# Kernel tuning notes

Measured on AMD Instinct MI355X. Metric: run time of the kernel, lower is better.

## Reference

```python
import jax, jax.numpy as jnp
import numpy as np
from jax import lax

# ---- module hyperparams (match init_kwargs and mamba_ssm Mamba2 defaults) ----
D_MODEL = 768
D_STATE = 64
D_CONV = 4
EXPAND = 2
HEADDIM = 64  # Mamba2 default
D_INNER = EXPAND * D_MODEL          # 1536
NHEADS = D_INNER // HEADDIM         # 24
NGROUPS = 1
CONV_DIM = D_INNER + 2 * NGROUPS * D_STATE          # 1664
D_IN_PROJ = 2 * D_INNER + 2 * NGROUPS * D_STATE + NHEADS  # 3224
BSZ, SEQ = 2, 512
EPS = 1e-5


def setup_inputs() -> dict:
    key = jax.random.key(0)
    ks = jax.random.split(key, 12)
    def n(k, shape, s):
        return jax.random.normal(k, shape, jnp.float32) * s
    x = n(ks[0], (BSZ, SEQ, D_MODEL), 1.0)
    in_proj_w = n(ks[1], (D_IN_PROJ, D_MODEL), D_MODEL ** -0.5)
    conv_w = n(ks[2], (CONV_DIM, D_CONV), D_CONV ** -0.5)
    conv_b = jnp.zeros((CONV_DIM,), jnp.float32)
    # dt_bias = softplus^{-1}(dt) with dt log-uniform in [1e-3, 1e-1] (Mamba2 init)
    dt = jnp.exp(jax.random.uniform(ks[3], (NHEADS,), jnp.float32,
                                    minval=np.log(1e-3), maxval=np.log(1e-1)))
    dt_bias = dt + jnp.log(-jnp.expm1(-dt))
    A_log = jnp.log(jax.random.uniform(ks[4], (NHEADS,), jnp.float32, minval=1.0, maxval=16.0))
    D_param = jnp.ones((NHEADS,), jnp.float32)
    norm_w = jnp.ones((D_INNER,), jnp.float32)
    out_proj_w = n(ks[5], (D_MODEL, D_INNER), D_INNER ** -0.5)
    ln1_w = jnp.ones((D_MODEL,), jnp.float32); ln1_b = jnp.zeros((D_MODEL,), jnp.float32)
    ln2_w = jnp.ones((D_MODEL,), jnp.float32); ln2_b = jnp.zeros((D_MODEL,), jnp.float32)
    ff_w1 = n(ks[6], (4 * D_MODEL, D_MODEL), D_MODEL ** -0.5)
    ff_b1 = jnp.zeros((4 * D_MODEL,), jnp.float32)
    ff_w2 = n(ks[7], (D_MODEL, 4 * D_MODEL), (4 * D_MODEL) ** -0.5)
    ff_b2 = jnp.zeros((D_MODEL,), jnp.float32)
    return dict(x=x, in_proj_w=in_proj_w, conv_w=conv_w, conv_b=conv_b,
                dt_bias=dt_bias, A_log=A_log, D_param=D_param, norm_w=norm_w,
                out_proj_w=out_proj_w, ln1_w=ln1_w, ln1_b=ln1_b,
                ln2_w=ln2_w, ln2_b=ln2_b, ff_w1=ff_w1, ff_b1=ff_b1,
                ff_w2=ff_w2, ff_b2=ff_b2)


def layernorm(x, w, b):
    mu = jnp.mean(x, -1, keepdims=True)
    xc = x - mu
    var = jnp.mean(xc * xc, -1, keepdims=True)
    return xc * lax.rsqrt(var + EPS) * w + b


def mamba2(xn, in_proj_w, conv_w, conv_b, dt_bias, A_log, D_param, norm_w, out_proj_w):
    b, l, _ = xn.shape
    zxbcdt = xn @ in_proj_w.T  # [b, l, D_IN_PROJ]
    z = zxbcdt[..., :D_INNER]
    xBC = zxbcdt[..., D_INNER:D_INNER + CONV_DIM]
    dt = zxbcdt[..., D_INNER + CONV_DIM:]
    # causal depthwise conv over time on xBC
    xc = lax.conv_general_dilated(xBC.transpose(0, 2, 1), conv_w[:, None, :], (1,),
                                  [(D_CONV - 1, 0)], dimension_numbers=('NCH', 'OIH', 'NCH'),
                                  feature_group_count=CONV_DIM)
    xBC = jax.nn.silu((xc + conv_b[None, :, None]).transpose(0, 2, 1))
    xs = xBC[..., :D_INNER].reshape(b, l, NHEADS, HEADDIM)
    Bm = xBC[..., D_INNER:D_INNER + D_STATE]   # [b, l, n]  (ngroups=1)
    Cm = xBC[..., D_INNER + D_STATE:]          # [b, l, n]
    dt = jax.nn.softplus(dt + dt_bias)         # [b, l, h]
    dA = jnp.exp(dt * (-jnp.exp(A_log)))       # [b, l, h]
    dBx = jnp.einsum('blh,bln,blhp->blhpn', dt, Bm, xs)
    def step(h, inp):
        dA_t, dBx_t = inp                      # [b,h], [b,h,p,n]
        h = dA_t[:, :, None, None] * h + dBx_t
        return h, h
    _, hs = lax.scan(step, jnp.zeros((b, NHEADS, HEADDIM, D_STATE), xn.dtype),
                     (dA.transpose(1, 0, 2), dBx.transpose(1, 0, 2, 3, 4)))
    y = jnp.einsum('lbhpn,bln->blhp', hs, Cm) + D_param[None, None, :, None] * xs
    y = y.reshape(b, l, D_INNER) * jax.nn.silu(z)   # gated RMSNorm (norm_before_gate=False)
    y = y * lax.rsqrt(jnp.mean(y * y, -1, keepdims=True) + EPS) * norm_w
    return y @ out_proj_w.T


def reference(x, in_proj_w, conv_w, conv_b, dt_bias, A_log, D_param, norm_w,
              out_proj_w, ln1_w, ln1_b, ln2_w, ln2_b, ff_w1, ff_b1, ff_w2, ff_b2):
    residual = x
    xn = layernorm(x, ln1_w, ln1_b)
    mp = (in_proj_w, conv_w, conv_b, dt_bias, A_log, D_param, norm_w, out_proj_w)
    out_f = mamba2(xn, *mp)
    out_b = jnp.flip(mamba2(jnp.flip(xn, 1), *mp), 1)
    m = layernorm(out_f + out_b, ln2_w, ln2_b)
    ff = jax.nn.gelu(m @ ff_w1.T + ff_b1, approximate=False) @ ff_w2.T + ff_b2
    return ff + residual
```

## Files before the change

### kernel.cpp

```cpp
#include <hip/hip_runtime.h>
#include <hip/hip_bf16.h>
#include <math.h>

#define SEQ     512
#define BSZ     2
#define ROWS    (BSZ*SEQ)
#define DMODEL  768
#define DINNER  1536
#define DSTATE  64
#define NHEADS  24
#define HEADDIM 64
#define CONVDIM 1664
#define DINPROJ 3224
#define DFF     3072
#define EPSF    1e-5f

typedef __attribute__((ext_vector_type(8))) short s16x8;
typedef __attribute__((ext_vector_type(4))) float f32x4;

__device__ __forceinline__ float b2f(const __hip_bfloat16 v){ return __bfloat162float(v); }
__device__ __forceinline__ __hip_bfloat16 f2b(float v){ return __float2bfloat16(v); }
__device__ __forceinline__ ushort f2bu(float v){
  union { __hip_bfloat16 b; ushort u; } c; c.b = __float2bfloat16(v); return c.u;
}
__device__ __forceinline__ float u2f(ushort u){ return __uint_as_float(((uint)u) << 16); }

__device__ __forceinline__ void gload16(const void* g, void* l){
  __builtin_amdgcn_global_load_lds((__attribute__((address_space(1))) const void*)g,
                                   (__attribute__((address_space(3))) void*)l, 16, 0, 0);
}

__device__ __forceinline__ float block_sum256(float v, float* sh){
  #pragma unroll
  for (int off = 32; off > 0; off >>= 1) v += __shfl_down(v, off, 64);
  int w = threadIdx.x >> 6;
  if ((threadIdx.x & 63) == 0) sh[w] = v;
  __syncthreads();
  float t = sh[0] + sh[1] + sh[2] + sh[3];
  __syncthreads();
  return t;
}

__global__ __launch_bounds__(256) void zerof_kernel(float* out, int n){
  int i = blockIdx.x*256 + threadIdx.x;
  if (i < n) out[i] = 0.f;
}

__global__ __launch_bounds__(256) void w2b_kernel(const float* __restrict__ w,
    __hip_bfloat16* __restrict__ o, int n)
{
  int i = (blockIdx.x*256 + threadIdx.x) << 2;
  if (i >= n) return;
  float4 f = *(const float4*)(w + i);
  ushort4 u = make_ushort4(f2bu(f.x), f2bu(f.y), f2bu(f.z), f2bu(f.w));
  *(ushort4*)((ushort*)o + i) = u;
}

__global__ __launch_bounds__(256) void ln_kernel(const float* __restrict__ in,
    const float* __restrict__ w, const float* __restrict__ b,
    __hip_bfloat16* __restrict__ out)
{
  __shared__ float sh[4];
  const int row = blockIdx.x;
  const float* xr = in + (size_t)row * DMODEL;
  float v[3]; float s = 0.f;
  #pragma unroll
  for (int i = 0; i < 3; i++){ int c = threadIdx.x + i*256; v[i] = xr[c]; s += v[i]; }
  s = block_sum256(s, sh);
  float mu = s * (1.f/DMODEL);
  float s2 = 0.f;
  #pragma unroll
  for (int i = 0; i < 3; i++){ float d = v[i]-mu; s2 += d*d; }
  s2 = block_sum256(s2, sh);
  float rs = rsqrtf(s2*(1.f/DMODEL) + EPSF);
  #pragma unroll
  for (int i = 0; i < 3; i++){
    int c = threadIdx.x + i*256;
    out[(size_t)row*DMODEL + c] = f2b((v[i]-mu)*rs*w[c] + b[c]);
  }
}

__device__ __forceinline__ s16x8 ld_frag(const ushort* p){
  union { ushort4 h[2]; s16x8 v; } u;
  u.h[0] = *(const ushort4*)(p);
  u.h[1] = *(const ushort4*)(p + 4);
  return u.v;
}

template<typename CTy, int KS>
__global__ __launch_bounds__(256) void gemm_bb64(const __hip_bfloat16* __restrict__ A_,
    const __hip_bfloat16* __restrict__ B_, CTy* __restrict__ C, int M, int N, int K)
{
  __shared__ __align__(16) ushort As[2][64][64];
  __shared__ __align__(16) ushort Bs[2][64][64];
  const int tid  = threadIdx.x;
  const int lane = tid & 63, wave = tid >> 6;
  const int wr = wave >> 1, wc = wave & 1;
  const int n0 = blockIdx.x * 64, m0 = blockIdx.y * 64;
  const int Kc   = K / KS;
  const int kbeg = blockIdx.z * Kc;
  const int srw  = lane >> 3;
  const int scol = (((lane & 7) ^ srw) << 3);
  const int l15  = lane & 15;
  const int r7   = l15 & 7;
  const int c0   = lane >> 4;

  const ushort* Au = (const ushort*)A_;
  const ushort* Bu = (const ushort*)B_;

  f32x4 acc[2][2] = {};

  auto stage = [&](int bf, int k0){
    #pragma unroll
    for (int q = 0; q < 2; q++){
      int row = q*32 + wave*8 + srw;
      gload16(Au + (size_t)(m0 + row)*K + kbeg + k0 + scol, &As[bf][q*32 + wave*8][0]);
      int nr = n0 + row; if (nr > N-1) nr = N-1;
      gload16(Bu + (size_t)nr*K + kbeg + k0 + scol, &Bs[bf][q*32 + wave*8][0]);
    }
  };

  stage(0, 0);
  __syncthreads();
  int cur = 0;
  for (int k0 = 0; k0 < Kc; k0 += 64){
    if (k0 + 64 < Kc) stage(cur ^ 1, k0 + 64);
    #pragma unroll
    for (int t = 0; t < 2; t++){
      const int fc = (((t*4 + c0) ^ r7) << 3);
      s16x8 a0 = ld_frag(&As[cur][wr*32      + l15][fc]);
      s16x8 a1 = ld_frag(&As[cur][wr*32 + 16 + l15][fc]);
      s16x8 b0 = ld_frag(&Bs[cur][wc*32      + l15][fc]);
      s16x8 b1 = ld_frag(&Bs[cur][wc*32 + 16 + l15][fc]);
      acc[0][0] = __builtin_amdgcn_mfma_f32_16x16x32_bf16(a0, b0, acc[0][0], 0, 0, 0);
      acc[0][1] = __builtin_amdgcn_mfma_f32_16x16x32_bf16(a0, b1, acc[0][1], 0, 0, 0);
      acc[1][0] = __builtin_amdgcn_mfma_f32_16x16x32_bf16(a1, b0, acc[1][0], 0, 0, 0);
      acc[1][1] = __builtin_amdgcn_mfma_f32_16x16x32_bf16(a1, b1, acc[1][1], 0, 0, 0);
    }
    __syncthreads();
    cur ^= 1;
  }

  const int crow = (lane >> 4) * 4;
  #pragma unroll
  for (int i = 0; i < 2; i++){
    #pragma unroll
    for (int j = 0; j < 2; j++){
      int col = n0 + wc*32 + j*16 + l15;
      if (col < N){
        #pragma unroll
        for (int q = 0; q < 4; q++){
          int rowg = m0 + wr*32 + i*16 + crow + q;
          if constexpr (KS > 1) atomicAdd(&C[(size_t)rowg*N + col], acc[i][j][q]);
          else if constexpr (sizeof(CTy) == 4) C[(size_t)rowg*N + col] = acc[i][j][q];
          else C[(size_t)rowg*N + col] = (CTy)f2b(acc[i][j][q]);
        }
      }
    }
  }
}

template<typename CTy>
__global__ __launch_bounds__(256) void gemm_mfma(const __hip_bfloat16* __restrict__ A,
    const float* __restrict__ B, CTy* __restrict__ C, int M, int N, int K)
{
  __shared__ __align__(16) ushort As[64][72];
  __shared__ __align__(16) ushort Bs[64][72];
  const int tid  = threadIdx.x;
  const int lane = tid & 63, wave = tid >> 6;
  const int wr = wave >> 1, wc = wave & 1;
  const int n0 = blockIdx.x * 64, m0 = blockIdx.y * 64;
  const int sr = tid >> 2;
  const int sc = (tid & 3) * 16;
  const int l15 = lane & 15, lk = (lane >> 4) * 8;

  f32x4 acc[2][2] = {};

  const ushort* Au = (const ushort*)A;
  int nr = n0 + sr; if (nr > N-1) nr = N-1;

  for (int k0 = 0; k0 < K; k0 += 64){
    const ushort* ag = Au + (size_t)(m0 + sr)*K + (k0 + sc);
    ushort4 a0 = *(const ushort4*)(ag);
    ushort4 a1 = *(const ushort4*)(ag + 4);
    ushort4 a2 = *(const ushort4*)(ag + 8);
    ushort4 a3 = *(const ushort4*)(ag + 12);
    const float* bg = B + (size_t)nr*K + (k0 + sc);
    float4 f0 = *(const float4*)(bg);
    float4 f1 = *(const float4*)(bg + 4);
    float4 f2 = *(const float4*)(bg + 8);
    float4 f3 = *(const float4*)(bg + 12);
    ushort4 b0 = make_ushort4(f2bu(f0.x), f2bu(f0.y), f2bu(f0.z), f2bu(f0.w));
    ushort4 b1 = make_ushort4(f2bu(f1.x), f2bu(f1.y), f2bu(f1.z), f2bu(f1.w));
    ushort4 b2 = make_ushort4(f2bu(f2.x), f2bu(f2.y), f2bu(f2.z), f2bu(f2.w));
    ushort4 b3 = make_ushort4(f2bu(f3.x), f2bu(f3.y), f2bu(f3.z), f2bu(f3.w));

    __syncthreads();
    *(ushort4*)&As[sr][sc +  0] = a0;
    *(ushort4*)&As[sr][sc +  4] = a1;
    *(ushort4*)&As[sr][sc +  8] = a2;
    *(ushort4*)&As[sr][sc + 12] = a3;
    *(ushort4*)&Bs[sr][sc +  0] = b0;
    *(ushort4*)&Bs[sr][sc +  4] = b1;
    *(ushort4*)&Bs[sr][sc +  8] = b2;
    *(ushort4*)&Bs[sr][sc + 12] = b3;
    __syncthreads();

    #pragma unroll
    for (int kk = 0; kk < 64; kk += 32){
      s16x8 af0 = ld_frag(&As[wr*32      + l15][kk + lk]);
      s16x8 af1 = ld_frag(&As[wr*32 + 16 + l15][kk + lk]);
      s16x8 bf0 = ld_frag(&Bs[wc*32      + l15][kk + lk]);
      s16x8 bf1 = ld_frag(&Bs[wc*32 + 16 + l15][kk + lk]);
      acc[0][0] = __builtin_amdgcn_mfma_f32_16x16x32_bf16(af0, bf0, acc[0][0], 0, 0, 0);
      acc[0][1] = __builtin_amdgcn_mfma_f32_16x16x32_bf16(af0, bf1, acc[0][1], 0, 0, 0);
      acc[1][0] = __builtin_amdgcn_mfma_f32_16x16x32_bf16(af1, bf0, acc[1][0], 0, 0, 0);
      acc[1][1] = __builtin_amdgcn_mfma_f32_16x16x32_bf16(af1, bf1, acc[1][1], 0, 0, 0);
    }
  }

  const int crow = (lane >> 4) * 4;
  #pragma unroll
  for (int i = 0; i < 2; i++){
    #pragma unroll
    for (int j = 0; j < 2; j++){
      int col = n0 + wc*32 + j*16 + l15;
      if (col < N){
        #pragma unroll
        for (int q = 0; q < 4; q++){
          int rowg = m0 + wr*32 + i*16 + crow + q;
          if constexpr (sizeof(CTy) == 4) C[(size_t)rowg*N + col] = acc[i][j][q];
          else                            C[(size_t)rowg*N + col] = (CTy)f2b(acc[i][j][q]);
        }
      }
    }
  }
}

__global__ __launch_bounds__(256) void convdt_kernel(const __hip_bfloat16* __restrict__ zx,
    const float* __restrict__ cw, const float* __restrict__ cb,
    const float* __restrict__ dt_bias, const float* __restrict__ A_log,
    __hip_bfloat16* __restrict__ xconv, float* __restrict__ dtb, float* __restrict__ dab)
{
  const int tt = blockIdx.x, b = blockIdx.y, dir = blockIdx.z;
  size_t rowoff[4]; bool ok[4];
  #pragma unroll
  for (int k = 0; k < 4; k++){
    int s = tt - 3 + k;
    ok[k] = (s >= 0);
    int ss = ok[k] ? s : 0;
    int phys = dir ? (SEQ-1-ss) : ss;
    rowoff[k] = ((size_t)(b*SEQ + phys))*DINPROJ + DINNER;
  }
  __hip_bfloat16* outr = xconv + ((size_t)((dir*BSZ + b)*SEQ + tt))*CONVDIM;
  for (int c = threadIdx.x; c < CONVDIM; c += 256){
    float acc = cb[c];
    #pragma unroll
    for (int k = 0; k < 4; k++){
      if (ok[k]) acc += cw[c*4 + k] * b2f(zx[rowoff[k] + c]);
    }
    outr[c] = f2b(acc / (1.f + expf(-acc)));
  }
  if (dir == 0 && threadIdx.x < NHEADS){
    int h = threadIdx.x;
    size_t r = (size_t)b*SEQ + tt;
    float raw = b2f(zx[r*DINPROJ + (DINNER + CONVDIM) + h]) + dt_bias[h];
    float sp  = fmaxf(raw, 0.f) + log1pf(expf(-fabsf(raw)));
    dtb[r*NHEADS + h] = sp;
    dab[r*NHEADS + h] = expf(-sp * expf(A_log[h]));
  }
}

#define CT 16

__global__ __launch_bounds__(256) void scan_pass1(const __hip_bfloat16* __restrict__ xconv,
    const float* __restrict__ dtb, const float* __restrict__ dab,
    float* __restrict__ stateBuf, int CL)
{
  const int c = blockIdx.x, h = blockIdx.y, z = blockIdx.z;
  const int b = z & 1, dir = z >> 1;
  const int tid = threadIdx.x, lane = tid & 63, wave = tid >> 6, nb = wave * 16;
  __shared__ __align__(16) float Bc[CT][64], Xc[CT][64];
  __shared__ float dAc[CT], dtc[CT];
  float hreg[16];
  #pragma unroll
  for (int j = 0; j < 16; j++) hreg[j] = 0.f;
  const size_t dirbase = (size_t)z * SEQ;
  const int cstart = c * CL;

  const int ttl = tid >> 4, c4 = (tid & 15) << 2;

  for (int c0 = cstart; c0 < cstart + CL; c0 += CT){
    {
      const ushort* rowp = (const ushort*)xconv + (dirbase + c0 + ttl)*(size_t)CONVDIM;
      ushort4 bv = *(const ushort4*)(rowp + DINNER + c4);
      ushort4 xv = *(const ushort4*)(rowp + h*HEADDIM + c4);
      Bc[ttl][c4+0] = u2f(bv.x); Bc[ttl][c4+1] = u2f(bv.y);
      Bc[ttl][c4+2] = u2f(bv.z); Bc[ttl][c4+3] = u2f(bv.w);
      Xc[ttl][c4+0] = u2f(xv.x); Xc[ttl][c4+1] = u2f(xv.y);
      Xc[ttl][c4+2] = u2f(xv.z); Xc[ttl][c4+3] = u2f(xv.w);
    }
    if (tid < CT){
      int phys = dir ? (SEQ-1 - (c0 + tid)) : (c0 + tid);
      size_t r = (size_t)b*SEQ + phys;
      dAc[tid] = dab[r*NHEADS + h];
      dtc[tid] = dtb[r*NHEADS + h];
    }
    __syncthreads();

    #pragma unroll 4
    for (int tt = 0; tt < CT; tt++){
      float dA = dAc[tt];
      float dtx = dtc[tt] * Xc[tt][lane];
      const float4* Bq = (const float4*)&Bc[tt][nb];
      float4 B0 = Bq[0], B1 = Bq[1], B2 = Bq[2], B3 = Bq[3];
      hreg[ 0]=fmaf(dA,hreg[ 0],dtx*B0.x); hreg[ 1]=fmaf(dA,hreg[ 1],dtx*B0.y);
      hreg[ 2]=fmaf(dA,hreg[ 2],dtx*B0.z); hreg[ 3]=fmaf(dA,hreg[ 3],dtx*B0.w);
      hreg[ 4]=fmaf(dA,hreg[ 4],dtx*B1.x); hreg[ 5]=fmaf(dA,hreg[ 5],dtx*B1.y);
      hreg[ 6]=fmaf(dA,hreg[ 6],dtx*B1.z); hreg[ 7]=fmaf(dA,hreg[ 7],dtx*B1.w);
      hreg[ 8]=fmaf(dA,hreg[ 8],dtx*B2.x); hreg[ 9]=fmaf(dA,hreg[ 9],dtx*B2.y);
      hreg[10]=fmaf(dA,hreg[10],dtx*B2.z); hreg[11]=fmaf(dA,hreg[11],dtx*B2.w);
      hreg[12]=fmaf(dA,hreg[12],dtx*B3.x); hreg[13]=fmaf(dA,hreg[13],dtx*B3.y);
      hreg[14]=fmaf(dA,hreg[14],dtx*B3.z); hreg[15]=fmaf(dA,hreg[15],dtx*B3.w);
    }
    __syncthreads();
  }

  float* sp = stateBuf + (((size_t)c*4 + z)*NHEADS + h)*4096 + (size_t)lane*64 + nb;
  *(float4*)(sp +  0) = make_float4(hreg[ 0],hreg[ 1],hreg[ 2],hreg[ 3]);
  *(float4*)(sp +  4) = make_float4(hreg[ 4],hreg[ 5],hreg[ 6],hreg[ 7]);
  *(float4*)(sp +  8) = make_float4(hreg[ 8],hreg[ 9],hreg[10],hreg[11]);
  *(float4*)(sp + 12) = make_float4(hreg[12],hreg[13],hreg[14],hreg[15]);
}

__global__ __launch_bounds__(256) void scan_fixup(const float* __restrict__ dab,
    float* __restrict__ stateBuf, int NC, int CL)
{
  const int h = blockIdx.x, z = blockIdx.y;
  const int b = z & 1, dir = z >> 1;
  const int tid = threadIdx.x;
  __shared__ float sdA[SEQ];
  __shared__ float P[8];
  for (int i = tid; i < SEQ; i += 256){
    int phys = dir ? (SEQ-1-i) : i;
    sdA[i] = dab[((size_t)b*SEQ + phys)*NHEADS + h];
  }
  __syncthreads();
  if (tid < NC){
    float p = 1.f;
    for (int i = 0; i < CL; i++) p *= sdA[tid*CL + i];
    P[tid] = p;
  }
  __syncthreads();

  float hrun[16], Lcur[16];
  #pragma unroll
  for (int j = 0; j < 16; j++) hrun[j] = 0.f;
  {
    const float* s0 = stateBuf + ((size_t)z*NHEADS + h)*4096 + (size_t)tid*16;
    #pragma unroll
    for (int j = 0; j < 16; j++) Lcur[j] = s0[j];
  }
  for (int c = 1; c < NC; c++){
    float Pp = P[c-1];
    float hnew[16];
    #pragma unroll
    for (int j = 0; j < 16; j++) hnew[j] = fmaf(Pp, hrun[j], Lcur[j]);
    float* sc = stateBuf + (((size_t)c*4 + z)*NHEADS + h)*4096 + (size_t)tid*16;
    if (c < NC-1){
      #pragma unroll
      for (int j = 0; j < 16; j++) Lcur[j] = sc[j];
    }
    #pragma unroll
    for (int j = 0; j < 16; j++) sc[j] = hnew[j];
    #pragma unroll
    for (int j = 0; j < 16; j++) hrun[j] = hnew[j];
  }
}

__global__ __launch_bounds__(256) void scan_pass2(const __hip_bfloat16* __restrict__ xconv,
    const __hip_bfloat16* __restrict__ zx, const float* __restrict__ dtb,
    const float* __restrict__ dab, const float* __restrict__ Dp,
    const float* __restrict__ stateBuf, __hip_bfloat16* __restrict__ yg, int CL)
{
  const int c = blockIdx.x, h = blockIdx.y, z = blockIdx.z;
  const int b = z & 1, dir = z >> 1;
  const int tid = threadIdx.x, lane = tid & 63, wave = tid >> 6, nb = wave * 16;
  __shared__ __align__(16) float Bc[CT][64], Cc[CT][64], Xc[CT][64];
  __shared__ __align__(16) float Yp[4][CT][64];
  __shared__ float dAc[CT], dtc[CT];
  float hreg[16];
  if (c == 0){
    #pragma unroll
    for (int j = 0; j < 16; j++) hreg[j] = 0.f;
  } else {
    const float* sp = stateBuf + (((size_t)c*4 + z)*NHEADS + h)*4096 + (size_t)lane*64 + nb;
    float4 s0 = *(const float4*)(sp+0), s1 = *(const float4*)(sp+4);
    float4 s2 = *(const float4*)(sp+8), s3 = *(const float4*)(sp+12);
    hreg[ 0]=s0.x; hreg[ 1]=s0.y; hreg[ 2]=s0.z; hreg[ 3]=s0.w;
    hreg[ 4]=s1.x; hreg[ 5]=s1.y; hreg[ 6]=s1.z; hreg[ 7]=s1.w;
    hreg[ 8]=s2.x; hreg[ 9]=s2.y; hreg[10]=s2.z; hreg[11]=s2.w;
    hreg[12]=s3.x; hreg[13]=s3.y; hreg[14]=s3.z; hreg[15]=s3.w;
  }
  const float Dh = Dp[h];
  const size_t dirbase = (size_t)z * SEQ;
  const int cstart = c * CL;
  const int ttl = tid >> 4, c4 = (tid & 15) << 2;

  for (int c0 = cstart; c0 < cstart + CL; c0 += CT){
    {
      const ushort* rowp = (const ushort*)xconv + (dirbase + c0 + ttl)*(size_t)CONVDIM;
      ushort4 bv = *(const ushort4*)(rowp + DINNER + c4);
      ushort4 cv = *(const ushort4*)(rowp + DINNER + DSTATE + c4);
      ushort4 xv = *(const ushort4*)(rowp + h*HEADDIM + c4);
      Bc[ttl][c4+0] = u2f(bv.x); Bc[ttl][c4+1] = u2f(bv.y);
      Bc[ttl][c4+2] = u2f(bv.z); Bc[ttl][c4+3] = u2f(bv.w);
      Cc[ttl][c4+0] = u2f(cv.x); Cc[ttl][c4+1] = u2f(cv.y);
      Cc[ttl][c4+2] = u2f(cv.z); Cc[ttl][c4+3] = u2f(cv.w);
      Xc[ttl][c4+0] = u2f(xv.x); Xc[ttl][c4+1] = u2f(xv.y);
      Xc[ttl][c4+2] = u2f(xv.z); Xc[ttl][c4+3] = u2f(xv.w);
    }
    if (tid < CT){
      int phys = dir ? (SEQ-1 - (c0 + tid)) : (c0 + tid);
      size_t r = (size_t)b*SEQ + phys;
      dAc[tid] = dab[r*NHEADS + h];
      dtc[tid] = dtb[r*NHEADS + h];
    }
    __syncthreads();

    #pragma unroll 4
    for (int tt = 0; tt < CT; tt++){
      float dA = dAc[tt];
      float dtx = dtc[tt] * Xc[tt][lane];
      const float4* Bq = (const float4*)&Bc[tt][nb];
      const float4* Cq = (const float4*)&Cc[tt][nb];
      float4 B0 = Bq[0], B1 = Bq[1], B2 = Bq[2], B3 = Bq[3];
      float4 C0 = Cq[0], C1 = Cq[1], C2 = Cq[2], C3 = Cq[3];
      float y0 = 0.f, y1 = 0.f, y2 = 0.f, y3 = 0.f;
      hreg[ 0]=fmaf(dA,hreg[ 0],dtx*B0.x); y0=fmaf(hreg[ 0],C0.x,y0);
      hreg[ 1]=fmaf(dA,hreg[ 1],dtx*B0.y); y1=fmaf(hreg[ 1],C0.y,y1);
      hreg[ 2]=fmaf(dA,hreg[ 2],dtx*B0.z); y2=fmaf(hreg[ 2],C0.z,y2);
      hreg[ 3]=fmaf(dA,hreg[ 3],dtx*B0.w); y3=fmaf(hreg[ 3],C0.w,y3);
      hreg[ 4]=fmaf(dA,hreg[ 4],dtx*B1.x); y0=fmaf(hreg[ 4],C1.x,y0);
      hreg[ 5]=fmaf(dA,hreg[ 5],dtx*B1.y); y1=fmaf(hreg[ 5],C1.y,y1);
      hreg[ 6]=fmaf(dA,hreg[ 6],dtx*B1.z); y2=fmaf(hreg[ 6],C1.z,y2);
      hreg[ 7]=fmaf(dA,hreg[ 7],dtx*B1.w); y3=fmaf(hreg[ 7],C1.w,y3);
      hreg[ 8]=fmaf(dA,hreg[ 8],dtx*B2.x); y0=fmaf(hreg[ 8],C2.x,y0);
      hreg[ 9]=fmaf(dA,hreg[ 9],dtx*B2.y); y1=fmaf(hreg[ 9],C2.y,y1);
      hreg[10]=fmaf(dA,hreg[10],dtx*B2.z); y2=fmaf(hreg[10],C2.z,y2);
      hreg[11]=fmaf(dA,hreg[11],dtx*B2.w); y3=fmaf(hreg[11],C2.w,y3);
      hreg[12]=fmaf(dA,hreg[12],dtx*B3.x); y0=fmaf(hreg[12],C3.x,y0);
      hreg[13]=fmaf(dA,hreg[13],dtx*B3.y); y1=fmaf(hreg[13],C3.y,y1);
      hreg[14]=fmaf(dA,hreg[14],dtx*B3.z); y2=fmaf(hreg[14],C3.z,y2);
      hreg[15]=fmaf(dA,hreg[15],dtx*B3.w); y3=fmaf(hreg[15],C3.w,y3);
      Yp[wave][tt][lane] = (y0+y1) + (y2+y3);
    }
    __syncthreads();

    for (int i = tid; i < CT*64; i += 256){
      int tl = i >> 6, p = i & 63;
      float y = Yp[0][tl][p] + Yp[1][tl][p] + Yp[2][tl][p] + Yp[3][tl][p]
              + Dh * Xc[tl][p];
      int phys = dir ? (SEQ-1 - (c0 + tl)) : (c0 + tl);
      size_t r = (size_t)b*SEQ + phys;
      float zval = b2f(zx[r*DINPROJ + h*HEADDIM + p]);
      float sil  = zval / (1.f + expf(-zval));
      yg[((size_t)dir*ROWS + r)*DINNER + h*HEADDIM + p] = f2b(y * sil);
    }
    __syncthreads();
  }
}

__global__ __launch_bounds__(256) void rmscomb_kernel(const __hip_bfloat16* __restrict__ yg,
    const float* __restrict__ nw, __hip_bfloat16* __restrict__ u)
{
  __shared__ float sh[4];
  const int row = blockIdx.x;
  const __hip_bfloat16* yf = yg + (size_t)row*DINNER;
  const __hip_bfloat16* yb = yg + (size_t)(ROWS + row)*DINNER;
  float vf[6], vb[6]; float sf = 0.f, sb = 0.f;
  #pragma unroll
  for (int i = 0; i < 6; i++){
    int c = threadIdx.x + i*256;
    vf[i] = b2f(yf[c]); sf += vf[i]*vf[i];
    vb[i] = b2f(yb[c]); sb += vb[i]*vb[i];
  }
  sf = block_sum256(sf, sh);
  sb = block_sum256(sb, sh);
  float rf = rsqrtf(sf*(1.f/DINNER) + EPSF);
  float rb = rsqrtf(sb*(1.f/DINNER) + EPSF);
  #pragma unroll
  for (int i = 0; i < 6; i++){
    int c = threadIdx.x + i*256;
    u[(size_t)row*DINNER + c] = f2b((vf[i]*rf + vb[i]*rb) * nw[c]);
  }
}

__global__ __launch_bounds__(256) void ln2_kernel(const float* __restrict__ in,
    const float* __restrict__ w, const float* __restrict__ b,
    __hip_bfloat16* __restrict__ out)
{
  __shared__ float sh[4];
  const int row = blockIdx.x;
  const float* xr = in + (size_t)row * DMODEL;
  float v[3]; float s = 0.f;
  #pragma unroll
  for (int i = 0; i < 3; i++){ int c = threadIdx.x + i*256; v[i] = xr[c]; s += v[i]; }
  s = block_sum256(s, sh);
  float mu = s * (1.f/DMODEL);
  float s2 = 0.f;
  #pragma unroll
  for (int i = 0; i < 3; i++){ float d = v[i]-mu; s2 += d*d; }
  s2 = block_sum256(s2, sh);
  float rs = rsqrtf(s2*(1.f/DMODEL) + EPSF);
  #pragma unroll
  for (int i = 0; i < 3; i++){
    int c = threadIdx.x + i*256;
    out[(size_t)row*DMODEL + c] = f2b((v[i]-mu)*rs*w[c] + b[c]);
  }
}

__global__ __launch_bounds__(256) void gelu_kernel(const __hip_bfloat16* __restrict__ g,
    const float* __restrict__ b1, __hip_bfloat16* __restrict__ out)
{
  size_t idx = (size_t)blockIdx.x*256 + threadIdx.x;
  int c = (int)(idx % DFF);
  float v = b2f(g[idx]) + b1[c];
  out[idx] = f2b(0.5f * v * (1.f + erff(v * 0.70710678118654752f)));
}

__global__ __launch_bounds__(256) void final_kernel(const float* __restrict__ f,
    const float* __restrict__ bias, const float* __restrict__ x,
    float* __restrict__ out)
{
  size_t idx = (size_t)blockIdx.x*256 + threadIdx.x;
  int c = (int)(idx % DMODEL);
  out[idx] = f[idx] + bias[c] + x[idx];
}

extern "C" void kernel_launch(void* const* d_in, const int* in_sizes, int n_in,
                              void* d_out, int out_size, void* d_ws, size_t ws_size,
                              hipStream_t stream)
{
  float* out = (float*)d_out;

  const size_t NEED = 19906560;
  if (ws_size < NEED || n_in < 17){
    zerof_kernel<<<(out_size + 255)/256, 256, 0, stream>>>(out, out_size);
    return;
  }

  const float* x       = (const float*)d_in[0];
  const float* in_proj_w = (const float*)d_in[1];
  const float* conv_w  = (const float*)d_in[2];
  const float* conv_b  = (const float*)d_in[3];
  const float* dt_bias = (const float*)d_in[4];
  const float* A_log   = (const float*)d_in[5];
  const float* D_param = (const float*)d_in[6];
  const float* norm_w  = (const float*)d_in[7];
  const float* out_proj_w = (const float*)d_in[8];
  const float* ln1_w   = (const float*)d_in[9];
  const float* ln1_b   = (const float*)d_in[10];
  const float* ln2_w   = (const float*)d_in[11];
  const float* ln2_b   = (const float*)d_in[12];
  const float* ff_w1   = (const float*)d_in[13];
  const float* ff_b1   = (const float*)d_in[14];
  const float* ff_w2   = (const float*)d_in[15];
  const float* ff_b2   = (const float*)d_in[16];

  char* ws = (char*)d_ws;
  __hip_bfloat16* zx  = (__hip_bfloat16*)(ws + 0);
  __hip_bfloat16* xn  = (__hip_bfloat16*)(ws + 6602752);
  float*          dtb = (float*)(ws + 6602752);
  float*          dab = (float*)(ws + 6701056);
  __hip_bfloat16* xcv = (__hip_bfloat16*)(ws + 6799360);
  __hip_bfloat16* yg  = (__hip_bfloat16*)(ws + 13615104);
  __hip_bfloat16* u   = (__hip_bfloat16*)(ws + 0);
  float*          mo  = (float*)(ws + 3145728);
  __hip_bfloat16* mb  = (__hip_bfloat16*)(ws + 0);
  __hip_bfloat16* g   = (__hip_bfloat16*)(ws + 6799360);
  __hip_bfloat16* gb  = (__hip_bfloat16*)(ws + 13615104);
  float*          fo  = (float*)(ws + 0);

  const size_t WBB = 4952064;
  const size_t CHB = 1572864;
  size_t rem = ws_size - NEED;
  bool useWB = (rem >= WBB);
  __hip_bfloat16* wb = (__hip_bfloat16*)(ws + NEED);
  if (useWB) rem -= WBB;
  int NC = 1;
  if      (rem >= 8*CHB) NC = 8;
  else if (rem >= 4*CHB) NC = 4;
  else if (rem >= 2*CHB) NC = 2;
  float* stateBuf = (float*)(ws + NEED + (useWB ? WBB : 0));
  const int CL = SEQ / NC;

  ln_kernel<<<ROWS, 256, 0, stream>>>(x, ln1_w, ln1_b, xn);
  if (useWB){
    w2b_kernel<<<(DINPROJ*DMODEL/4 + 255)/256, 256, 0, stream>>>(in_proj_w, wb, DINPROJ*DMODEL);
    gemm_bb64<__hip_bfloat16,1><<<dim3((DINPROJ+63)/64, ROWS/64), 256, 0, stream>>>(xn, wb, zx, ROWS, DINPROJ, DMODEL);
  } else {
    gemm_mfma<<<dim3((DINPROJ+63)/64, ROWS/64), 256, 0, stream>>>(xn, in_proj_w, zx, ROWS, DINPROJ, DMODEL);
  }
  convdt_kernel<<<dim3(SEQ, BSZ, 2), 256, 0, stream>>>(zx, conv_w, conv_b, dt_bias, A_log, xcv, dtb, dab);
  if (NC > 1){
    scan_pass1<<<dim3(NC-1, NHEADS, 4), 256, 0, stream>>>(xcv, dtb, dab, stateBuf, CL);
    scan_fixup<<<dim3(NHEADS, 4), 256, 0, stream>>>(dab, stateBuf, NC, CL);
  }
  scan_pass2<<<dim3(NC, NHEADS, 4), 256, 0, stream>>>(xcv, zx, dtb, dab, D_param, stateBuf, yg, CL);
  rmscomb_kernel<<<ROWS, 256, 0, stream>>>(yg, norm_w, u);
  if (useWB){
    w2b_kernel<<<(DMODEL*DINNER/4 + 255)/256, 256, 0, stream>>>(out_proj_w, wb, DMODEL*DINNER);
    zerof_kernel<<<(ROWS*DMODEL + 255)/256, 256, 0, stream>>>(mo, ROWS*DMODEL);
    gemm_bb64<float,2><<<dim3(DMODEL/64, ROWS/64, 2), 256, 0, stream>>>(u, wb, mo, ROWS, DMODEL, DINNER);
  } else {
    gemm_mfma<<<dim3(DMODEL/64, ROWS/64), 256, 0, stream>>>(u, out_proj_w, mo, ROWS, DMODEL, DINNER);
  }
  ln2_kernel<<<ROWS, 256, 0, stream>>>(mo, ln2_w, ln2_b, mb);
  if (useWB){
    w2b_kernel<<<(DFF*DMODEL/4 + 255)/256, 256, 0, stream>>>(ff_w1, wb, DFF*DMODEL);
    gemm_bb64<__hip_bfloat16,1><<<dim3(DFF/64, ROWS/64), 256, 0, stream>>>(mb, wb, g, ROWS, DFF, DMODEL);
  } else {
    gemm_mfma<<<dim3(DFF/64, ROWS/64), 256, 0, stream>>>(mb, ff_w1, g, ROWS, DFF, DMODEL);
  }
  gelu_kernel<<<(ROWS*DFF)/256, 256, 0, stream>>>(g, ff_b1, gb);
  if (useWB){
    w2b_kernel<<<(DMODEL*DFF/4 + 255)/256, 256, 0, stream>>>(ff_w2, wb, DMODEL*DFF);
    zerof_kernel<<<(ROWS*DMODEL + 255)/256, 256, 0, stream>>>(fo, ROWS*DMODEL);
    gemm_bb64<float,4><<<dim3(DMODEL/64, ROWS/64, 4), 256, 0, stream>>>(gb, wb, fo, ROWS, DMODEL, DFF);
  } else {
    gemm_mfma<<<dim3(DMODEL/64, ROWS/64), 256, 0, stream>>>(gb, ff_w2, fo, ROWS, DMODEL, DFF);
  }
  final_kernel<<<(ROWS*DMODEL)/256, 256, 0, stream>>>(fo, ff_b2, x, out);
}
```

Before: 283.7 us.

## Batch weight conversion, fuse GELU epilogue, replace split-K atomics with partial buffers

All four weight matrices are now converted to bf16 in a single kernel launch instead of four separate ones. GELU and bias are fused into the FF1 GEMM epilogue, which removes the separate gelu kernel and the intermediate round trip. Split-K GEMMs write per-slice partial buffers that are summed in ln2 and the final kernel, replacing the zeroing kernels and atomicAdd. The conv, scan-output and final kernels are also vectorised. The cost is a larger workspace requirement, and if the workspace is too small the code falls back to the slow path.

```diff
diff --git a/kernel.cpp b/kernel.cpp
--- a/kernel.cpp
+++ b/kernel.cpp
@@ -46,14 +46,22 @@
   if (i < n) out[i] = 0.f;
 }
 
-__global__ __launch_bounds__(256) void w2b_kernel(const float* __restrict__ w,
-    __hip_bfloat16* __restrict__ o, int n)
+__global__ __launch_bounds__(256) void w2ball_kernel(const float* __restrict__ w0,
+    const float* __restrict__ w1, const float* __restrict__ w2,
+    const float* __restrict__ w3, ushort* __restrict__ o,
+    int n0, int n1, int n2, int n3)
 {
   int i = (blockIdx.x*256 + threadIdx.x) << 2;
-  if (i >= n) return;
-  float4 f = *(const float4*)(w + i);
+  int total = n0 + n1 + n2 + n3;
+  if (i >= total) return;
+  const float* s; int off;
+  if      (i < n0)          { s = w0; off = i; }
+  else if (i < n0+n1)       { s = w1; off = i - n0; }
+  else if (i < n0+n1+n2)    { s = w2; off = i - n0 - n1; }
+  else                      { s = w3; off = i - n0 - n1 - n2; }
+  float4 f = *(const float4*)(s + off);
   ushort4 u = make_ushort4(f2bu(f.x), f2bu(f.y), f2bu(f.z), f2bu(f.w));
-  *(ushort4*)((ushort*)o + i) = u;
+  *(ushort4*)(o + i) = u;
 }
 
 __global__ __launch_bounds__(256) void ln_kernel(const float* __restrict__ in,
@@ -87,9 +95,10 @@
   return u.v;
 }
 
-template<typename CTy, int KS>
+template<typename CTy, int KS, int EPI>
 __global__ __launch_bounds__(256) void gemm_bb64(const __hip_bfloat16* __restrict__ A_,
-    const __hip_bfloat16* __restrict__ B_, CTy* __restrict__ C, int M, int N, int K)
+    const __hip_bfloat16* __restrict__ B_, CTy* __restrict__ C,
+    const float* __restrict__ bias, int M, int N, int K)
 {
   __shared__ __align__(16) ushort As[2][64][64];
   __shared__ __align__(16) ushort Bs[2][64][64];
@@ -141,6 +150,7 @@
     cur ^= 1;
   }
 
+  CTy* Cz = C + (size_t)blockIdx.z * M * N;
   const int crow = (lane >> 4) * 4;
   #pragma unroll
   for (int i = 0; i < 2; i++){
@@ -151,9 +161,14 @@
         #pragma unroll
         for (int q = 0; q < 4; q++){
           int rowg = m0 + wr*32 + i*16 + crow + q;
-          if constexpr (KS > 1) atomicAdd(&C[(size_t)rowg*N + col], acc[i][j][q]);
-          else if constexpr (sizeof(CTy) == 4) C[(size_t)rowg*N + col] = acc[i][j][q];
-          else C[(size_t)rowg*N + col] = (CTy)f2b(acc[i][j][q]);
+          if constexpr (EPI == 1){
+            float v = acc[i][j][q] + bias[col];
+            Cz[(size_t)rowg*N + col] = (CTy)f2b(0.5f * v * (1.f + erff(v * 0.70710678118654752f)));
+          } else if constexpr (sizeof(CTy) == 4){
+            Cz[(size_t)rowg*N + col] = acc[i][j][q];
+          } else {
+            Cz[(size_t)rowg*N + col] = (CTy)f2b(acc[i][j][q]);
+          }
         }
       }
     }
@@ -243,23 +258,55 @@
     __hip_bfloat16* __restrict__ xconv, float* __restrict__ dtb, float* __restrict__ dab)
 {
   const int tt = blockIdx.x, b = blockIdx.y, dir = blockIdx.z;
-  size_t rowoff[4]; bool ok[4];
-  #pragma unroll
-  for (int k = 0; k < 4; k++){
-    int s = tt - 3 + k;
-    ok[k] = (s >= 0);
-    int ss = ok[k] ? s : 0;
-    int phys = dir ? (SEQ-1-ss) : ss;
-    rowoff[k] = ((size_t)(b*SEQ + phys))*DINPROJ + DINNER;
-  }
-  __hip_bfloat16* outr = xconv + ((size_t)((dir*BSZ + b)*SEQ + tt))*CONVDIM;
-  for (int c = threadIdx.x; c < CONVDIM; c += 256){
-    float acc = cb[c];
+  const int c8 = threadIdx.x * 8;
+  if (c8 < CONVDIM){
+    size_t rowoff[4]; bool ok[4];
     #pragma unroll
     for (int k = 0; k < 4; k++){
-      if (ok[k]) acc += cw[c*4 + k] * b2f(zx[rowoff[k] + c]);
-    }
-    outr[c] = f2b(acc / (1.f + expf(-acc)));
+      int s = tt - 3 + k;
+      ok[k] = (s >= 0);
+      int ss = ok[k] ? s : 0;
+      int phys = dir ? (SEQ-1-ss) : ss;
+      rowoff[k] = ((size_t)(b*SEQ + phys))*DINPROJ + DINNER + c8;
+    }
+    float acc[8];
+    {
+      float4 cb0 = *(const float4*)(cb + c8);
+      float4 cb1 = *(const float4*)(cb + c8 + 4);
+      acc[0]=cb0.x; acc[1]=cb0.y; acc[2]=cb0.z; acc[3]=cb0.w;
+      acc[4]=cb1.x; acc[5]=cb1.y; acc[6]=cb1.z; acc[7]=cb1.w;
+    }
+    float wv[8][4];
+    #pragma unroll
+    for (int j = 0; j < 8; j++){
+      float4 w4 = *(const float4*)(cw + (size_t)(c8 + j)*4);
+      wv[j][0]=w4.x; wv[j][1]=w4.y; wv[j][2]=w4.z; wv[j][3]=w4.w;
+    }
+    const ushort* zu = (const ushort*)zx;
+    #pragma unroll
+    for (int k = 0; k < 4; k++){
+      if (ok[k]){
+        ushort4 v0 = *(const ushort4*)(zu + rowoff[k]);
+        ushort4 v1 = *(const ushort4*)(zu + rowoff[k] + 4);
+        acc[0] = fmaf(wv[0][k], u2f(v0.x), acc[0]);
+        acc[1] = fmaf(wv[1][k], u2f(v0.y), acc[1]);
+        acc[2] = fmaf(wv[2][k], u2f(v0.z), acc[2]);
+        acc[3] = fmaf(wv[3][k], u2f(v0.w), acc[3]);
+        acc[4] = fmaf(wv[4][k], u2f(v1.x), acc[4]);
+        acc[5] = fmaf(wv[5][k], u2f(v1.y), acc[5]);
+        acc[6] = fmaf(wv[6][k], u2f(v1.z), acc[6]);
+        acc[7] = fmaf(wv[7][k], u2f(v1.w), acc[7]);
+      }
+    }
+    ushort* outr = (ushort*)xconv + ((size_t)((dir*BSZ + b)*SEQ + tt))*CONVDIM + c8;
+    ushort o[8];
+    #pragma unroll
+    for (int j = 0; j < 8; j++){
+      float s = acc[j] / (1.f + expf(-acc[j]));
+      o[j] = f2bu(s);
+    }
+    *(ushort4*)(outr)     = make_ushort4(o[0],o[1],o[2],o[3]);
+    *(ushort4*)(outr + 4) = make_ushort4(o[4],o[5],o[6],o[7]);
   }
   if (dir == 0 && threadIdx.x < NHEADS){
     int h = threadIdx.x;
@@ -457,15 +504,30 @@
     }
     __syncthreads();
 
-    for (int i = tid; i < CT*64; i += 256){
-      int tl = i >> 6, p = i & 63;
-      float y = Yp[0][tl][p] + Yp[1][tl][p] + Yp[2][tl][p] + Yp[3][tl][p]
-              + Dh * Xc[tl][p];
+    {
+      int tl = tid >> 4, p4 = (tid & 15) << 2;
+      float4 ya = *(const float4*)&Yp[0][tl][p4];
+      float4 yb4 = *(const float4*)&Yp[1][tl][p4];
+      float4 yc = *(const float4*)&Yp[2][tl][p4];
+      float4 yd = *(const float4*)&Yp[3][tl][p4];
+      float4 xv = *(const float4*)&Xc[tl][p4];
       int phys = dir ? (SEQ-1 - (c0 + tl)) : (c0 + tl);
       size_t r = (size_t)b*SEQ + phys;
-      float zval = b2f(zx[r*DINPROJ + h*HEADDIM + p]);
-      float sil  = zval / (1.f + expf(-zval));
-      yg[((size_t)dir*ROWS + r)*DINNER + h*HEADDIM + p] = f2b(y * sil);
+      const ushort* zp = (const ushort*)zx + r*DINPROJ + h*HEADDIM + p4;
+      ushort4 zv = *(const ushort4*)zp;
+      float zf[4] = { u2f(zv.x), u2f(zv.y), u2f(zv.z), u2f(zv.w) };
+      float yv[4] = { ya.x+yb4.x+yc.x+yd.x + Dh*xv.x,
+                      ya.y+yb4.y+yc.y+yd.y + Dh*xv.y,
+                      ya.z+yb4.z+yc.z+yd.z + Dh*xv.z,
+                      ya.w+yb4.w+yc.w+yd.w + Dh*xv.w };
+      ushort o[4];
+      #pragma unroll
+      for (int j = 0; j < 4; j++){
+        float sil = zf[j] / (1.f + expf(-zf[j]));
+        o[j] = f2bu(yv[j] * sil);
+      }
+      ushort* op = (ushort*)yg + ((size_t)dir*ROWS + r)*DINNER + h*HEADDIM + p4;
+      *(ushort4*)op = make_ushort4(o[0],o[1],o[2],o[3]);
     }
     __syncthreads();
   }
@@ -496,16 +558,23 @@
   }
 }
 
+template<int NP>
 __global__ __launch_bounds__(256) void ln2_kernel(const float* __restrict__ in,
-    const float* __restrict__ w, const float* __restrict__ b,
+    size_t pstride, const float* __restrict__ w, const float* __restrict__ b,
     __hip_bfloat16* __restrict__ out)
 {
   __shared__ float sh[4];
   const int row = blockIdx.x;
-  const float* xr = in + (size_t)row * DMODEL;
   float v[3]; float s = 0.f;
   #pragma unroll
-  for (int i = 0; i < 3; i++){ int c = threadIdx.x + i*256; v[i] = xr[c]; s += v[i]; }
+  for (int i = 0; i < 3; i++){
+    int c = threadIdx.x + i*256;
+    size_t idx = (size_t)row*DMODEL + c;
+    float t = 0.f;
+    #pragma unroll
+    for (int p = 0; p < NP; p++) t += in[p*pstride + idx];
+    v[i] = t; s += t;
+  }
   s = block_sum256(s, sh);
   float mu = s * (1.f/DMODEL);
   float s2 = 0.f;
@@ -529,13 +598,22 @@
   out[idx] = f2b(0.5f * v * (1.f + erff(v * 0.70710678118654752f)));
 }
 
+template<int NP>
 __global__ __launch_bounds__(256) void final_kernel(const float* __restrict__ f,
-    const float* __restrict__ bias, const float* __restrict__ x,
+    size_t pstride, const float* __restrict__ bias, const float* __restrict__ x,
     float* __restrict__ out)
 {
-  size_t idx = (size_t)blockIdx.x*256 + threadIdx.x;
-  int c = (int)(idx % DMODEL);
-  out[idx] = f[idx] + bias[c] + x[idx];
+  size_t i4 = ((size_t)blockIdx.x*256 + threadIdx.x) << 2;
+  int c = (int)(i4 % DMODEL);
+  float4 bv = *(const float4*)(bias + c);
+  float4 xv = *(const float4*)(x + i4);
+  float4 s = make_float4(bv.x+xv.x, bv.y+xv.y, bv.z+xv.z, bv.w+xv.w);
+  #pragma unroll
+  for (int p = 0; p < NP; p++){
+    float4 fv = *(const float4*)(f + p*pstride + i4);
+    s.x += fv.x; s.y += fv.y; s.z += fv.z; s.w += fv.w;
+  }
+  *(float4*)(out + i4) = s;
 }
 
 extern "C" void kernel_launch(void* const* d_in, const int* in_sizes, int n_in,
@@ -582,23 +660,37 @@
   __hip_bfloat16* gb  = (__hip_bfloat16*)(ws + 13615104);
   float*          fo  = (float*)(ws + 0);
 
-  const size_t WBB = 4952064;
-  const size_t CHB = 1572864;
+  const size_t WBALL = 16748544;
+  const size_t PARTS = 12582912;
+  const size_t CHB   = 1572864;
+  const size_t PSTRIDE = (size_t)ROWS * DMODEL;
+  const int WN_IN = DINPROJ*DMODEL;
+  const int WN_OUT = DMODEL*DINNER;
+  const int WN_F1 = DFF*DMODEL;
+  const int WN_F2 = DMODEL*DFF;
+
   size_t rem = ws_size - NEED;
-  bool useWB = (rem >= WBB);
-  __hip_bfloat16* wb = (__hip_bfloat16*)(ws + NEED);
-  if (useWB) rem -= WBB;
+  bool fast = (rem >= WBALL + PARTS);
+  ushort* wb    = (ushort*)(ws + NEED);
+  float*  parts = (float*) (ws + NEED + WBALL);
+  size_t scanoff = NEED + (fast ? (WBALL + PARTS) : 0);
+  size_t srem = ws_size - scanoff;
   int NC = 1;
-  if      (rem >= 8*CHB) NC = 8;
-  else if (rem >= 4*CHB) NC = 4;
-  else if (rem >= 2*CHB) NC = 2;
-  float* stateBuf = (float*)(ws + NEED + (useWB ? WBB : 0));
+  if      (srem >= 8*CHB) NC = 8;
+  else if (srem >= 4*CHB) NC = 4;
+  else if (srem >= 2*CHB) NC = 2;
+  float* stateBuf = (float*)(ws + scanoff);
   const int CL = SEQ / NC;
 
   ln_kernel<<<ROWS, 256, 0, stream>>>(x, ln1_w, ln1_b, xn);
-  if (useWB){
-    w2b_kernel<<<(DINPROJ*DMODEL/4 + 255)/256, 256, 0, stream>>>(in_proj_w, wb, DINPROJ*DMODEL);
-    gemm_bb64<__hip_bfloat16,1><<<dim3((DINPROJ+63)/64, ROWS/64), 256, 0, stream>>>(xn, wb, zx, ROWS, DINPROJ, DMODEL);
+  if (fast){
+    int total4 = (WN_IN + WN_OUT + WN_F1 + WN_F2) / 4;
+    w2ball_kernel<<<(total4 + 255)/256, 256, 0, stream>>>(in_proj_w, out_proj_w,
+        ff_w1, ff_w2, wb, WN_IN, WN_OUT, WN_F1, WN_F2);
+  }
+  if (fast){
+    gemm_bb64<__hip_bfloat16,1,0><<<dim3((DINPROJ+63)/64, ROWS/64), 256, 0, stream>>>(
+        xn, (const __hip_bfloat16*)wb, zx, nullptr, ROWS, DINPROJ, DMODEL);
   } else {
     gemm_mfma<<<dim3((DINPROJ+63)/64, ROWS/64), 256, 0, stream>>>(xn, in_proj_w, zx, ROWS, DINPROJ, DMODEL);
   }
@@ -609,27 +701,27 @@
   }
   scan_pass2<<<dim3(NC, NHEADS, 4), 256, 0, stream>>>(xcv, zx, dtb, dab, D_param, stateBuf, yg, CL);
   rmscomb_kernel<<<ROWS, 256, 0, stream>>>(yg, norm_w, u);
-  if (useWB){
-    w2b_kernel<<<(DMODEL*DINNER/4 + 255)/256, 256, 0, stream>>>(out_proj_w, wb, DMODEL*DINNER);
-    zerof_kernel<<<(ROWS*DMODEL + 255)/256, 256, 0, stream>>>(mo, ROWS*DMODEL);
-    gemm_bb64<float,2><<<dim3(DMODEL/64, ROWS/64, 2), 256, 0, stream>>>(u, wb, mo, ROWS, DMODEL, DINNER);
+  if (fast){
+    gemm_bb64<float,2,0><<<dim3(DMODEL/64, ROWS/64, 2), 256, 0, stream>>>(
+        u, (const __hip_bfloat16*)(wb + WN_IN), parts, nullptr, ROWS, DMODEL, DINNER);
+    ln2_kernel<2><<<ROWS, 256, 0, stream>>>(parts, PSTRIDE, ln2_w, ln2_b, mb);
   } else {
     gemm_mfma<<<dim3(DMODEL/64, ROWS/64), 256, 0, stream>>>(u, out_proj_w, mo, ROWS, DMODEL, DINNER);
-  }
-  ln2_kernel<<<ROWS, 256, 0, stream>>>(mo, ln2_w, ln2_b, mb);
-  if (useWB){
-    w2b_kernel<<<(DFF*DMODEL/4 + 255)/256, 256, 0, stream>>>(ff_w1, wb, DFF*DMODEL);
-    gemm_bb64<__hip_bfloat16,1><<<dim3(DFF/64, ROWS/64), 256, 0, stream>>>(mb, wb, g, ROWS, DFF, DMODEL);
+    ln2_kernel<1><<<ROWS, 256, 0, stream>>>(mo, 0, ln2_w, ln2_b, mb);
+  }
+  if (fast){
+    gemm_bb64<__hip_bfloat16,1,1><<<dim3(DFF/64, ROWS/64), 256, 0, stream>>>(
+        mb, (const __hip_bfloat16*)(wb + WN_IN + WN_OUT), gb, ff_b1, ROWS, DFF, DMODEL);
   } else {
     gemm_mfma<<<dim3(DFF/64, ROWS/64), 256, 0, stream>>>(mb, ff_w1, g, ROWS, DFF, DMODEL);
-  }
-  gelu_kernel<<<(ROWS*DFF)/256, 256, 0, stream>>>(g, ff_b1, gb);
-  if (useWB){
-    w2b_kernel<<<(DMODEL*DFF/4 + 255)/256, 256, 0, stream>>>(ff_w2, wb, DMODEL*DFF);
-    zerof_kernel<<<(ROWS*DMODEL + 255)/256, 256, 0, stream>>>(fo, ROWS*DMODEL);
-    gemm_bb64<float,4><<<dim3(DMODEL/64, ROWS/64, 4), 256, 0, stream>>>(gb, wb, fo, ROWS, DMODEL, DFF);
+    gelu_kernel<<<(ROWS*DFF)/256, 256, 0, stream>>>(g, ff_b1, gb);
+  }
+  if (fast){
+    gemm_bb64<float,4,0><<<dim3(DMODEL/64, ROWS/64, 4), 256, 0, stream>>>(
+        gb, (const __hip_bfloat16*)(wb + WN_IN + WN_OUT + WN_F1), parts, nullptr, ROWS, DMODEL, DFF);
+    final_kernel<4><<<(ROWS*DMODEL/4)/256, 256, 0, stream>>>(parts, PSTRIDE, ff_b2, x, out);
   } else {
     gemm_mfma<<<dim3(DMODEL/64, ROWS/64), 256, 0, stream>>>(gb, ff_w2, fo, ROWS, DMODEL, DFF);
-  }
-  final_kernel<<<(ROWS*DMODEL)/256, 256, 0, stream>>>(fo, ff_b2, x, out);
-}
+    final_kernel<1><<<(ROWS*DMODEL/4)/256, 256, 0, stream>>>(fo, 0, ff_b2, x, out);
+  }
+}
```

New measurement: 251.2 us. 11.4% less time.
